# Kernel optimization log

Measured on AMD Instinct MI355X. Metric: run time of the kernel, lower is better.

The kernel has to match this reference:

```python
import jax, jax.numpy as jnp
import numpy as np

C = 10          # max gap (in timesteps) between spikes within one cluster
NEG = -1e30     # finite stand-in for -inf (safe under where/vjp)


def setup_inputs() -> dict:
    key = jax.random.key(0)
    k1, k2, k3 = jax.random.split(key, 3)
    B, N, T = 128, 256, 1024
    vmem = jax.random.normal(k1, (B, N, T), dtype=jnp.float32)
    vlastmem = jax.random.normal(k2, (B, N, T), dtype=jnp.float32)
    labels = jax.random.randint(k3, (B,), 0, N)
    return {"vmem": vmem, "vlastmem": vlastmem, "labels": labels}


def _loss_and_spikes(vmem, labels, C):
    B, N, T = vmem.shape
    BN = B * N
    v = vmem.reshape(BN, T)
    # labels_t[b, n] = 1 iff labels[b] == n  (one-hot over neurons)
    target = (labels[:, None] == jnp.arange(N)[None, :]).astype(vmem.dtype).reshape(BN)

    spike = v >= 0                                  # [BN, T]
    s = spike.astype(jnp.int32)
    cs = jnp.cumsum(s, axis=-1)                     # inclusive prefix sums of spikes
    csp = jnp.pad(cs, ((0, 0), (C + 1, 0)))         # csp[:, t] = cs[t - C - 1] (0 if oob)
    win = csp[:, C:C + T] - csp[:, :T]              # #spikes in window [t-C, t-1]
    # a spike starts a new cluster iff no spike within the previous C steps
    is_start = spike & (win == 0)
    cid = jnp.cumsum(is_start.astype(jnp.int32), axis=-1) - 1   # cluster id at each t
    num_cluster = cid[:, -1] + 1                    # [BN] (0 if no spikes)

    # clusters are at least C+1 apart, so at most K per row
    K = (T - 1) // (C + 1) + 1
    cidc = jnp.clip(cid, 0, K - 1)
    gid = (jnp.arange(BN)[:, None] * K + cidc).reshape(-1)      # global segment ids

    # per-cluster spike count, first spike time, last spike time
    sizes = jax.ops.segment_sum(s.reshape(-1), gid, num_segments=BN * K).reshape(BN, K)
    tb = jnp.broadcast_to(jnp.arange(T), (BN, T))
    first = jax.ops.segment_min(jnp.where(spike, tb, T).reshape(-1), gid,
                                num_segments=BN * K).reshape(BN, K)
    last = jax.ops.segment_max(jnp.where(spike, tb, -1).reshape(-1), gid,
                               num_segments=BN * K).reshape(BN, K)

    # smallest cluster (argmin over end-beg == spike count; first occurrence on ties)
    valid = jnp.arange(K)[None, :] < num_cluster[:, None]
    idx = jnp.argmin(jnp.where(valid, sizes, T + 1), axis=-1)   # [BN]
    f = jnp.take_along_axis(first, idx[:, None], axis=-1)       # [BN, 1]
    l = jnp.take_along_axis(last, idx[:, None], axis=-1)
    span = (tb >= f) & (tb <= l)
    max_span = jnp.max(jnp.where(span, v, NEG), axis=-1)        # max v over smallest cluster
    max_all = jnp.max(v, axis=-1)                               # max v (no-spike case)

    nc = num_cluster.astype(vmem.dtype)
    # target > nc  <=> target==1 and no spikes  -> loss -= max(v) (mask is all zero)
    # target < nc  -> loss += max(v over smallest cluster span)
    contrib = jnp.where(target > nc, -max_all,
                        jnp.where(target < nc, max_span, jnp.zeros_like(max_all)))
    loss = jnp.sum(contrib)
    spike_output = nc.reshape(B, N)
    return loss, spike_output


def reference(vmem, vlastmem, labels):
    # vlastmem is unused by the original forward; kept for signature fidelity
    return _loss_and_spikes(vmem, labels, C)
```

## Files before the change

### kernel.cpp

```cpp
#include <hip/hip_runtime.h>
#include <cstdint>

#define T_DIM 1024
#define NW 16
#define C_GAP 10
#define NEGF (-1e30f)

__device__ __forceinline__ int wmin_i(int v) {
    #pragma unroll
    for (int s = 32; s >= 1; s >>= 1) v = min(v, __shfl_xor(v, s));
    return v;
}
__device__ __forceinline__ int wmax_i(int v) {
    #pragma unroll
    for (int s = 32; s >= 1; s >>= 1) v = max(v, __shfl_xor(v, s));
    return v;
}
__device__ __forceinline__ int wsum_i(int v) {
    #pragma unroll
    for (int s = 32; s >= 1; s >>= 1) v += __shfl_xor(v, s);
    return v;
}
__device__ __forceinline__ float wmax_f(float v) {
    #pragma unroll
    for (int s = 32; s >= 1; s >>= 1) v = fmaxf(v, __shfl_xor(v, s));
    return v;
}

__global__ __launch_bounds__(256) void stca_rows(const float* __restrict__ vmem,
                                                 const int* __restrict__ labels,
                                                 float* __restrict__ out,
                                                 float* __restrict__ partial,
                                                 int N)
{
    __shared__ float red[4];

    const int wid  = threadIdx.x >> 6;
    const int lane = threadIdx.x & 63;
    const int row  = (blockIdx.x << 2) | wid;
    const int b    = row / N;
    const int n    = row - b * N;

    const float* vrow = vmem + (size_t)row * T_DIM;

    float val[NW];
    float maxall = NEGF;
    #pragma unroll
    for (int w = 0; w < NW; ++w) {
        val[w] = vrow[(w << 6) + lane];
        maxall = fmaxf(maxall, val[w]);
    }
    maxall = wmax_f(maxall);

    uint64_t m[NW];
    #pragma unroll
    for (int w = 0; w < NW; ++w)
        m[w] = __ballot(val[w] >= 0.0f);

    int nclust = 0;
    uint64_t mw = 0, sw = 0;
    const int myw = lane & 15;
    #pragma unroll
    for (int w = 0; w < NW; ++w) {
        uint64_t P = (w == 0) ? 0ull : m[w - 1];
        uint64_t win = 0;
        #pragma unroll
        for (int sft = 1; sft <= C_GAP; ++sft)
            win |= (m[w] << sft) | (P >> (64 - sft));
        uint64_t st = m[w] & ~win;
        nclust += __popcll(st);
        if (myw == w) { mw = m[w]; sw = st; }
    }

    const float target = (labels[b] == n) ? 1.0f : 0.0f;
    float contrib = 0.0f;

    if (nclust == 0) {
        if (target > 0.5f) contrib = -maxall;
    } else {
        const int base = myw << 6;

        int cand = sw ? (base + (__ffsll((unsigned long long)sw) - 1)) : T_DIM;
        int s = wmin_i(cand);

        int min_size = 1 << 30, min_f = 0, min_l = 0;
        while (s < T_DIM) {
            int d = s - base;
            uint64_t gt = (d < 0) ? ~0ull : ((d >= 63) ? 0ull : ~((2ull << d) - 1));
            uint64_t cb = sw & gt;
            int cn = cb ? (base + (__ffsll((unsigned long long)cb) - 1)) : T_DIM;
            int e = wmin_i(cn);

            int lo = s - base; lo = lo < 0 ? 0 : (lo > 64 ? 64 : lo);
            int hi = e - base; hi = hi < 0 ? 0 : (hi > 64 ? 64 : hi);
            uint64_t below_hi = (hi >= 64) ? ~0ull : ((1ull << hi) - 1ull);
            uint64_t below_lo = (lo >= 64) ? ~0ull : ((1ull << lo) - 1ull);
            uint64_t mb = mw & below_hi & ~below_lo;

            int size = wsum_i(__popcll(mb)) >> 2;
            int lp = mb ? (base + 63 - __clzll((long long)mb)) : -1;
            int last = wmax_i(lp);

            if (size < min_size) { min_size = size; min_f = s; min_l = last; }
            s = e;
        }

        float pmax = NEGF;
        #pragma unroll
        for (int w = 0; w < NW; ++w) {
            int t = (w << 6) + lane;
            pmax = fmaxf(pmax, (t >= min_f && t <= min_l) ? val[w] : NEGF);
        }
        pmax = wmax_f(pmax);

        if (target < (float)nclust) contrib = pmax;
    }

    if (lane == 0) {
        out[1 + row] = (float)nclust;
        red[wid] = contrib;
    }
    __syncthreads();
    if (threadIdx.x == 0)
        partial[blockIdx.x] = red[0] + red[1] + red[2] + red[3];
}

__global__ __launch_bounds__(256) void reduce_partials(const float* __restrict__ partial,
                                                       int n, float* __restrict__ out)
{
    float s = 0.0f;
    for (int i = threadIdx.x; i < n; i += 256) s += partial[i];
    #pragma unroll
    for (int k = 32; k >= 1; k >>= 1) s += __shfl_xor(s, k);
    __shared__ float red[4];
    const int wid = threadIdx.x >> 6, lane = threadIdx.x & 63;
    if (lane == 0) red[wid] = s;
    __syncthreads();
    if (threadIdx.x == 0) out[0] = red[0] + red[1] + red[2] + red[3];
}

extern "C" void kernel_launch(void* const* d_in, const int* in_sizes, int n_in,
                              void* d_out, int out_size, void* d_ws, size_t ws_size,
                              hipStream_t stream)
{
    const float* vmem   = (const float*)d_in[0];
    const int*   labels = (const int*)d_in[2];
    float* out     = (float*)d_out;
    float* partial = (float*)d_ws;

    const int BN = in_sizes[0] / T_DIM;
    const int B  = in_sizes[2];
    const int N  = BN / B;
    const int blocks = BN >> 2;

    stca_rows<<<blocks, 256, 0, stream>>>(vmem, labels, out, partial, N);
    reduce_partials<<<1, 256, 0, stream>>>(partial, blocks, out);
}
```

Baseline: 254.0 us.

## Use contiguous per-lane 16-element chunks with float4 loads and 32-bit spike masks

Each lane now loads 16 contiguous floats with float4 loads instead of 16 strided scalar loads. The spike mask becomes a per-lane 16-bit word, and cluster starts are found with a neighbour shuffle plus shift-OR doubling instead of 16 ballots and 64-bit window loops. The cluster-scan loop only runs when its result is needed (target < nclust). The partial reduction is also unrolled into four accumulators. The aim is fewer memory instructions and less ALU work per row, at the cost of rewriting the cluster-detection bit logic, which risks correctness errors at chunk boundaries.

```diff
diff --git a/kernel.cpp b/kernel.cpp
--- a/kernel.cpp
+++ b/kernel.cpp
@@ -2,7 +2,6 @@
 #include <cstdint>
 
 #define T_DIM 1024
-#define NW 16
 #define C_GAP 10
 #define NEGF (-1e30f)
 
@@ -40,80 +39,67 @@
     const int row  = (blockIdx.x << 2) | wid;
     const int b    = row / N;
     const int n    = row - b * N;
+    const int base = lane << 4;
 
-    const float* vrow = vmem + (size_t)row * T_DIM;
+    const float4* vrow = (const float4*)(vmem + (size_t)row * T_DIM);
 
-    float val[NW];
-    float maxall = NEGF;
+    union { float4 q[4]; float f[16]; } u;
     #pragma unroll
-    for (int w = 0; w < NW; ++w) {
-        val[w] = vrow[(w << 6) + lane];
-        maxall = fmaxf(maxall, val[w]);
-    }
-    maxall = wmax_f(maxall);
+    for (int c = 0; c < 4; ++c) u.q[c] = vrow[(lane << 2) + c];
 
-    uint64_t m[NW];
+    float maxlane = NEGF;
     #pragma unroll
-    for (int w = 0; w < NW; ++w)
-        m[w] = __ballot(val[w] >= 0.0f);
+    for (int j = 0; j < 16; ++j) maxlane = fmaxf(maxlane, u.f[j]);
 
-    int nclust = 0;
-    uint64_t mw = 0, sw = 0;
-    const int myw = lane & 15;
+    uint32_t x = 0;
     #pragma unroll
-    for (int w = 0; w < NW; ++w) {
-        uint64_t P = (w == 0) ? 0ull : m[w - 1];
-        uint64_t win = 0;
-        #pragma unroll
-        for (int sft = 1; sft <= C_GAP; ++sft)
-            win |= (m[w] << sft) | (P >> (64 - sft));
-        uint64_t st = m[w] & ~win;
-        nclust += __popcll(st);
-        if (myw == w) { mw = m[w]; sw = st; }
-    }
+    for (int j = 0; j < 16; ++j) x |= (u.f[j] >= 0.0f) ? (1u << j) : 0u;
 
+    uint32_t prev = __shfl_up(x, 1);
+    if (lane == 0) prev = 0u;
+    uint32_t z  = (x << 16) | prev;
+    uint32_t s1 = z << 1;
+    uint32_t s2 = s1 | (s1 << 1);
+    uint32_t s4 = s2 | (s2 << 2);
+    uint32_t s8 = s4 | (s4 << 4);
+    uint32_t sA = s8 | (s2 << 8);
+    uint32_t start = x & ~(sA >> 16) & 0xFFFFu;
+
+    const int nclust = wsum_i(__popc(start));
     const float target = (labels[b] == n) ? 1.0f : 0.0f;
+
     float contrib = 0.0f;
-
     if (nclust == 0) {
-        if (target > 0.5f) contrib = -maxall;
-    } else {
-        const int base = myw << 6;
-
-        int cand = sw ? (base + (__ffsll((unsigned long long)sw) - 1)) : T_DIM;
+        if (target > 0.5f) contrib = -wmax_f(maxlane);
+    } else if (target < (float)nclust) {
+        int cand = start ? (base + __ffs(start) - 1) : T_DIM;
         int s = wmin_i(cand);
 
         int min_size = 1 << 30, min_f = 0, min_l = 0;
         while (s < T_DIM) {
-            int d = s - base;
-            uint64_t gt = (d < 0) ? ~0ull : ((d >= 63) ? 0ull : ~((2ull << d) - 1));
-            uint64_t cb = sw & gt;
-            int cn = cb ? (base + (__ffsll((unsigned long long)cb) - 1)) : T_DIM;
-            int e = wmin_i(cn);
+            int rel = s - base;
+            uint32_t gt = (rel < 0) ? 0xFFFFu : ((rel >= 15) ? 0u : ((0xFFFFu << (rel + 1)) & 0xFFFFu));
+            uint32_t cb = start & gt;
+            int e = wmin_i(cb ? (base + __ffs(cb) - 1) : T_DIM);
 
-            int lo = s - base; lo = lo < 0 ? 0 : (lo > 64 ? 64 : lo);
-            int hi = e - base; hi = hi < 0 ? 0 : (hi > 64 ? 64 : hi);
-            uint64_t below_hi = (hi >= 64) ? ~0ull : ((1ull << hi) - 1ull);
-            uint64_t below_lo = (lo >= 64) ? ~0ull : ((1ull << lo) - 1ull);
-            uint64_t mb = mw & below_hi & ~below_lo;
+            int lo = s - base; lo = lo < 0 ? 0 : (lo > 16 ? 16 : lo);
+            int hi = e - base; hi = hi < 0 ? 0 : (hi > 16 ? 16 : hi);
+            uint32_t mb = x & ((1u << hi) - 1u) & ~((1u << lo) - 1u);
 
-            int size = wsum_i(__popcll(mb)) >> 2;
-            int lp = mb ? (base + 63 - __clzll((long long)mb)) : -1;
-            int last = wmax_i(lp);
+            int size = wsum_i(__popc(mb));
+            int last = wmax_i(mb ? (base + 31 - __clz(mb)) : -1);
 
             if (size < min_size) { min_size = size; min_f = s; min_l = last; }
             s = e;
         }
 
-        float pmax = NEGF;
+        float pm = NEGF;
         #pragma unroll
-        for (int w = 0; w < NW; ++w) {
-            int t = (w << 6) + lane;
-            pmax = fmaxf(pmax, (t >= min_f && t <= min_l) ? val[w] : NEGF);
+        for (int j = 0; j < 16; ++j) {
+            int t = base + j;
+            pm = (t >= min_f && t <= min_l) ? fmaxf(pm, u.f[j]) : pm;
         }
-        pmax = wmax_f(pmax);
-
-        if (target < (float)nclust) contrib = pmax;
+        contrib = wmax_f(pm);
     }
 
     if (lane == 0) {
@@ -128,8 +114,14 @@
 __global__ __launch_bounds__(256) void reduce_partials(const float* __restrict__ partial,
                                                        int n, float* __restrict__ out)
 {
-    float s = 0.0f;
-    for (int i = threadIdx.x; i < n; i += 256) s += partial[i];
+    float a0 = 0.f, a1 = 0.f, a2 = 0.f, a3 = 0.f;
+    for (int i = threadIdx.x; i < n; i += 1024) {
+        a0 += partial[i];
+        a1 += (i + 256 < n) ? partial[i + 256] : 0.f;
+        a2 += (i + 512 < n) ? partial[i + 512] : 0.f;
+        a3 += (i + 768 < n) ? partial[i + 768] : 0.f;
+    }
+    float s = (a0 + a1) + (a2 + a3);
     #pragma unroll
     for (int k = 32; k >= 1; k >>= 1) s += __shfl_xor(s, k);
     __shared__ float red[4];
```

Measured after the change: 247.0 us. 1.03x faster.
